# Performance work log

Measured on AMD Instinct MI355X. Metric: run time of the kernel, lower is better.

Reference implementation:

```python
import jax, jax.numpy as jnp
import numpy as np

GAZE_DIR = -1.0  # dataset != 'eyediap'
B, V, VM, LAT = 64, 5023, 3500, 556
D_IN = 3 * 224 * 224


def _skew(v):  # [B,3] -> [B,3,3]
    z = jnp.zeros_like(v[:, 0])
    return jnp.stack([
        jnp.stack([z, -v[:, 2], v[:, 1]], axis=1),
        jnp.stack([v[:, 2], z, -v[:, 0]], axis=1),
        jnp.stack([-v[:, 1], v[:, 0], z], axis=1)], axis=1)


def _axis_angle_to_matrix(aa):  # [B,3] -> [B,3,3], Rodrigues
    theta = jnp.linalg.norm(aa, axis=1, keepdims=True)
    axis = aa / jnp.maximum(theta, 1e-8)
    K = _skew(axis)
    s = jnp.sin(theta)[:, :, None]
    c = jnp.cos(theta)[:, :, None]
    return jnp.eye(3, dtype=aa.dtype) + s * K + (1.0 - c) * (K @ K)


def _find_gaze_R(init_gaze):  # rotation taking init_gaze -> [0,0,GAZE_DIR]
    a = init_gaze[:, 0, :]
    a = a / jnp.linalg.norm(a, axis=1, keepdims=True)
    b = jnp.broadcast_to(jnp.array([0.0, 0.0, GAZE_DIR], a.dtype), a.shape)
    v = jnp.cross(a, b)
    c = jnp.sum(a * b, axis=1)
    K = _skew(v)
    return jnp.eye(3, dtype=a.dtype) + K + (K @ K) * (1.0 / (1.0 + c + 1e-8))[:, None, None]


def _apply_eyeball_rotation(eyeball, centre, rot2):
    aa = jnp.concatenate([rot2, jnp.zeros_like(rot2[:, :1])], axis=1)
    R = _axis_angle_to_matrix(aa)
    return jnp.einsum('bvl,bli->bvi', eyeball - centre, R) + centre


def _forward(x, enc_W, enc_b, v_template, shape_basis, camera_parameters,
             landmarks, masked_landmarks, face_mask, lmask, rmask):
    b = x.shape[0]
    latent = x.reshape(b, -1) @ enc_W + enc_b  # encoder stub
    shape_p = latent[:, :400]
    face_rot = latent[:, 545:548]
    face_t = latent[:, 548:551]
    face_scale = latent[:, 551:552] + 1.0
    l_rot = latent[:, 552:554]
    r_rot = latent[:, 554:556]

    # FLAME shape model stub: template + linear blendshapes
    vert = v_template[None] + jnp.einsum('bs,svc->bvc', shape_p, shape_basis)
    vmean = vert.mean(axis=1, keepdims=True)
    vert = (jnp.einsum('bvl,bli->bvi', vert - vmean, _axis_angle_to_matrix(face_rot))
            * face_scale[:, :, None] + face_t[:, None, :])

    l_eye = vert[:, lmask]
    r_eye = vert[:, rmask]
    l_c = l_eye.mean(axis=1, keepdims=True)
    r_c = r_eye.mean(axis=1, keepdims=True)
    idx4 = landmarks[jnp.array([19, 22, 25, 28])]
    idx2 = landmarks[jnp.array([14, 18])]
    face_centre = (vert[:, idx4].mean(1) + vert[:, idx2].mean(1)) / 2.0

    l_init = vert[:, None, 4051] - l_c
    l_init = l_init / jnp.linalg.norm(l_init, axis=2, keepdims=True)
    r_init = vert[:, None, 4597] - r_c
    r_init = r_init / jnp.linalg.norm(r_init, axis=2, keepdims=True)

    le = jnp.einsum('bvl,bli->bvi', l_eye - l_c, _find_gaze_R(l_init)) + l_c
    re = jnp.einsum('bvl,bli->bvi', r_eye - r_c, _find_gaze_R(r_init)) + r_c
    le = _apply_eyeball_rotation(le, l_c, l_rot)
    re = _apply_eyeball_rotation(re, r_c, r_rot)
    # masks are disjoint: vert_no_eyes + vert_eyes == scatter back rotated eyes
    vert = vert.at[:, lmask].set(le).at[:, rmask].set(re)

    gdir = jnp.broadcast_to(jnp.array([0.0, 0.0, GAZE_DIR], vert.dtype), (b, 1, 3))
    zc = jnp.zeros((b, 1, 3), vert.dtype)
    left_gaze = _apply_eyeball_rotation(gdir, zc, l_rot)
    right_gaze = _apply_eyeball_rotation(gdir, zc, r_rot)

    lr_cross = jnp.cross(right_gaze, left_gaze, axis=2)
    A = jnp.concatenate([left_gaze, -right_gaze, lr_cross], axis=1).transpose(0, 2, 1)
    rhs = (r_c - l_c).transpose(0, 2, 1)
    sol = jnp.linalg.solve(A, rhs)  # [B,3,1]
    gp_l = l_c + sol[:, 0:1, :] * left_gaze
    gp_r = r_c + sol[:, 1:2, :] * right_gaze
    gp_mid = (gp_l + gp_r) / 2.0
    dist = jnp.linalg.norm(gp_l - gp_r, axis=2)  # [B,1]

    vmk = vert[:, face_mask]
    fl3d = vmk[:, masked_landmarks]
    # renderer stub: pinhole projection with [B,3,4] camera
    homog = jnp.concatenate([vmk, jnp.ones_like(vmk[..., :1])], axis=-1)
    p = jnp.einsum('bij,bvj->bvi', camera_parameters, homog)
    z = p[..., 2:3]
    zs = jnp.where(z >= 0, 1.0, -1.0) * jnp.maximum(jnp.abs(z), 1e-3)
    vert_img = jnp.concatenate([p[..., :2] / zs, z], axis=-1)

    dist_row = jnp.repeat(dist[:, :, None], 3, axis=2)  # [B,1,3]
    out = jnp.concatenate([
        vmk, vert_img, fl3d, l_c, r_c, face_centre[:, None, :],
        gp_l, gp_r, gp_mid,
        l_c + left_gaze * 1000.0, r_c + right_gaze * 1000.0,
        left_gaze, right_gaze, dist_row], axis=1)  # [B, 2*VM+68+11, 3]
    return out


def setup_inputs() -> dict:
    key = jax.random.key(0)
    ks = jax.random.split(key, 8)
    x = jax.random.normal(ks[0], (B, 3, 224, 224), jnp.float32)
    enc_W = jax.random.normal(ks[1], (D_IN, LAT), jnp.float32) * 1e-3
    enc_b = jax.random.normal(ks[2], (LAT,), jnp.float32) * 0.1
    v_template = jax.random.normal(ks[3], (V, 3), jnp.float32)
    shape_basis = jax.random.normal(ks[4], (400, V, 3), jnp.float32) * 0.01
    camera_parameters = jax.random.normal(ks[5], (B, 3, 4), jnp.float32)
    landmarks = jax.random.randint(ks[6], (68,), 0, VM)
    masked_landmarks = jax.random.randint(ks[7], (68,), 0, VM)
    face_mask = jnp.arange(VM)
    left_eyeball_mask = jnp.arange(3931, 4477)   # contains 4051
    right_eyeball_mask = jnp.arange(4477, 5023)  # contains 4597
    return {"x": x, "enc_W": enc_W, "enc_b": enc_b, "v_template": v_template,
            "shape_basis": shape_basis, "camera_parameters": camera_parameters,
            "landmarks": landmarks, "masked_landmarks": masked_landmarks,
            "face_mask": face_mask, "left_eyeball_mask": left_eyeball_mask,
            "right_eyeball_mask": right_eyeball_mask}


def reference(x, enc_W, enc_b, v_template, shape_basis, camera_parameters,
              landmarks, masked_landmarks, face_mask, left_eyeball_mask,
              right_eyeball_mask):
    return _forward(x, enc_W, enc_b, v_template, shape_basis, camera_parameters,
                    landmarks, masked_landmarks, face_mask, left_eyeball_mask,
                    right_eyeball_mask)
```

## Files before the change

kernel.cpp:

```cpp
#include <hip/hip_runtime.h>
#include <hip/hip_bf16.h>
#include <math.h>

#define B_    64
#define V_    5023
#define VM_   3500
#define LAT_  556
#define DIN_  150528
#define NS_   400
#define N2_   15069
#define ROWS_ 7079
#define LE0_  3931
#define NEYE_ 546

#define KC_   1024
#define KS_   32
#define NSUB_ (KC_/KS_)
#define SDW_  18
#define XSC_  64.0f
#define WSC_  4096.0f
#define OSC_  (1.0f/262144.0f)

#define WS_LATENT 0
#define WS_VERT0  35584
#define WS_VERT   1000000
#define WS_PB     1964416
#define PB_STRIDE 32

typedef _Float16 f16x8 __attribute__((ext_vector_type(8)));
typedef float    f32x4 __attribute__((ext_vector_type(4)));

union F16x8 { f16x8 v; unsigned int u[4]; _Float16 h[8]; };

static __device__ inline unsigned int packh(_Float16 a, _Float16 b) {
    union { _Float16 h; unsigned short u; } ca, cb;
    ca.h = a; cb.h = b;
    return (unsigned int)ca.u | ((unsigned int)cb.u << 16);
}

__global__ void k_init_latent(const float* __restrict__ enc_b,
                              float* __restrict__ latent) {
    int i = blockIdx.x * 256 + threadIdx.x;
    if (i < B_ * LAT_) latent[i] = enc_b[i % LAT_];
}

__global__ __launch_bounds__(256) void k_gemm(const float* __restrict__ x,
                                              const float* __restrict__ W,
                                              float* __restrict__ latent) {
    __shared__ __align__(16) unsigned int wt[2][2][64 * SDW_];
    const int tid = threadIdx.x;
    const int n0  = blockIdx.x * 64;
    const int k0  = blockIdx.y * KC_;
    const int sq   = tid & 15;
    const int skp  = tid >> 4;
    const int scol = n0 + sq * 4;
    const bool svalid = scol < LAT_;
    const int lane = tid & 63;
    const int w    = tid >> 6;
    const int wr   = w >> 1;
    const int wc   = w & 1;
    const int c16  = lane & 15;
    const int g    = lane >> 4;

    f32x4 acc[2][2] = {};
    float4 wv0, wv1;
    {
        const float* wp = W + (size_t)(k0 + 2 * skp) * LAT_ + scol;
        wv0 = svalid ? *(const float4*)wp : make_float4(0.f, 0.f, 0.f, 0.f);
        wv1 = svalid ? *(const float4*)(wp + LAT_) : make_float4(0.f, 0.f, 0.f, 0.f);
    }
    for (int s = 0; s < NSUB_; ++s) {
        const int db = s & 1;
        {
            float v0[4] = {wv0.x, wv0.y, wv0.z, wv0.w};
            float v1[4] = {wv1.x, wv1.y, wv1.z, wv1.w};
#pragma unroll
            for (int c = 0; c < 4; ++c) {
                float a = v0[c] * WSC_, b = v1[c] * WSC_;
                _Float16 h0 = (_Float16)a, h1 = (_Float16)b;
                _Float16 l0 = (_Float16)(a - (float)h0);
                _Float16 l1 = (_Float16)(b - (float)h1);
                wt[db][0][(sq * 4 + c) * SDW_ + skp] = packh(h0, h1);
                wt[db][1][(sq * 4 + c) * SDW_ + skp] = packh(l0, l1);
            }
        }
        if (s + 1 < NSUB_) {
            const float* wp = W + (size_t)(k0 + (s + 1) * KS_ + 2 * skp) * LAT_ + scol;
            wv0 = svalid ? *(const float4*)wp : make_float4(0.f, 0.f, 0.f, 0.f);
            wv1 = svalid ? *(const float4*)(wp + LAT_) : make_float4(0.f, 0.f, 0.f, 0.f);
        }
        __syncthreads();
        F16x8 ahi[2], alo[2];
#pragma unroll
        for (int rf = 0; rf < 2; ++rf) {
            const int row = 32 * wr + 16 * rf + c16;
            const float* xp = x + (size_t)row * DIN_ + k0 + s * KS_ + 8 * g;
            float4 a0 = *(const float4*)xp;
            float4 a1 = *(const float4*)(xp + 4);
            float av[8] = {a0.x, a0.y, a0.z, a0.w, a1.x, a1.y, a1.z, a1.w};
#pragma unroll
            for (int j = 0; j < 8; ++j) {
                float sv = av[j] * XSC_;
                _Float16 h = (_Float16)sv;
                ahi[rf].h[j] = h;
                alo[rf].h[j] = (_Float16)(sv - (float)h);
            }
        }
#pragma unroll
        for (int cf = 0; cf < 2; ++cf) {
            const int nl = 32 * wc + 16 * cf + c16;
            const unsigned int* ph = &wt[db][0][nl * SDW_ + 4 * g];
            const unsigned int* pl = &wt[db][1][nl * SDW_ + 4 * g];
            F16x8 bh, bl;
            uint2 t0 = *(const uint2*)ph;
            uint2 t1 = *(const uint2*)(ph + 2);
            bh.u[0] = t0.x; bh.u[1] = t0.y; bh.u[2] = t1.x; bh.u[3] = t1.y;
            uint2 u0 = *(const uint2*)pl;
            uint2 u1 = *(const uint2*)(pl + 2);
            bl.u[0] = u0.x; bl.u[1] = u0.y; bl.u[2] = u1.x; bl.u[3] = u1.y;
#pragma unroll
            for (int rf = 0; rf < 2; ++rf) {
                acc[rf][cf] = __builtin_amdgcn_mfma_f32_16x16x32_f16(ahi[rf].v, bh.v, acc[rf][cf], 0, 0, 0);
                acc[rf][cf] = __builtin_amdgcn_mfma_f32_16x16x32_f16(ahi[rf].v, bl.v, acc[rf][cf], 0, 0, 0);
                acc[rf][cf] = __builtin_amdgcn_mfma_f32_16x16x32_f16(alo[rf].v, bh.v, acc[rf][cf], 0, 0, 0);
            }
        }
    }
#pragma unroll
    for (int rf = 0; rf < 2; ++rf)
#pragma unroll
        for (int cf = 0; cf < 2; ++cf)
#pragma unroll
            for (int i = 0; i < 4; ++i) {
                int row = 32 * wr + 16 * rf + 4 * g + i;
                int col = n0 + 32 * wc + 16 * cf + c16;
                if (col < LAT_)
                    atomicAdd(&latent[row * LAT_ + col], acc[rf][cf][i] * OSC_);
            }
}

__global__ __launch_bounds__(256) void k_shape(const float* __restrict__ latent,
                                               const float* __restrict__ sb,
                                               const float* __restrict__ vt,
                                               float* __restrict__ vert0) {
    __shared__ float ps[16][64];
    __shared__ float bs[16][64];
    const int n0  = blockIdx.x * 64;
    const int tid = threadIdx.x;
    const int tb  = tid >> 4;
    const int tn  = tid & 15;
    const int lb  = tid >> 2;
    const int ls4 = (tid & 3) << 2;
    const int wss = tid >> 4;
    const int wn4 = (tid & 15) << 2;
    float acc[4][4];
#pragma unroll
    for (int j = 0; j < 4; ++j) {
        int nn = n0 + (tn << 2) + j;
        float v = (nn < N2_) ? vt[nn] : 0.f;
#pragma unroll
        for (int i = 0; i < 4; ++i) acc[i][j] = v;
    }
    for (int st = 0; st < NS_; st += 16) {
        float4 pv = *(const float4*)(latent + lb * LAT_ + st + ls4);
        float wv[4];
        int nn0 = n0 + wn4;
        if (nn0 + 3 < N2_) {
            float4 t = *(const float4*)(sb + (size_t)(st + wss) * N2_ + nn0);
            wv[0] = t.x; wv[1] = t.y; wv[2] = t.z; wv[3] = t.w;
        } else {
#pragma unroll
            for (int j = 0; j < 4; ++j) {
                int nn = nn0 + j;
                wv[j] = (nn < N2_) ? sb[(size_t)(st + wss) * N2_ + nn] : 0.f;
            }
        }
        __syncthreads();
        ps[ls4 + 0][lb] = pv.x;
        ps[ls4 + 1][lb] = pv.y;
        ps[ls4 + 2][lb] = pv.z;
        ps[ls4 + 3][lb] = pv.w;
#pragma unroll
        for (int j = 0; j < 4; ++j) bs[wss][wn4 + j] = wv[j];
        __syncthreads();
#pragma unroll
        for (int ss = 0; ss < 16; ++ss) {
            float4 av = *(const float4*)&ps[ss][tb << 2];
            float4 bv = *(const float4*)&bs[ss][tn << 2];
            float a[4] = {av.x, av.y, av.z, av.w};
            float b4[4] = {bv.x, bv.y, bv.z, bv.w};
#pragma unroll
            for (int i = 0; i < 4; ++i)
#pragma unroll
                for (int j = 0; j < 4; ++j)
                    acc[i][j] = fmaf(a[i], b4[j], acc[i][j]);
        }
    }
#pragma unroll
    for (int i = 0; i < 4; ++i) {
#pragma unroll
        for (int j = 0; j < 4; ++j) {
            int nn = n0 + (tn << 2) + j;
            if (nn < N2_) vert0[(size_t)((tb << 2) + i) * N2_ + nn] = acc[i][j];
        }
    }
}

__device__ inline void axis_angle(const float aa0, const float aa1, const float aa2,
                                  float R[9]) {
    float th  = sqrtf(aa0 * aa0 + aa1 * aa1 + aa2 * aa2);
    float inv = 1.0f / fmaxf(th, 1e-8f);
    float v0 = aa0 * inv, v1 = aa1 * inv, v2 = aa2 * inv;
    float s = sinf(th), c = cosf(th);
    float K[9] = {0.f, -v2, v1, v2, 0.f, -v0, -v1, v0, 0.f};
    float KK[9];
#pragma unroll
    for (int i = 0; i < 3; ++i)
#pragma unroll
        for (int j = 0; j < 3; ++j)
            KK[i * 3 + j] = K[i * 3 + 0] * K[0 * 3 + j] +
                            K[i * 3 + 1] * K[1 * 3 + j] +
                            K[i * 3 + 2] * K[2 * 3 + j];
    float omc = 1.0f - c;
#pragma unroll
    for (int i = 0; i < 9; ++i) R[i] = s * K[i] + omc * KK[i];
    R[0] += 1.f; R[4] += 1.f; R[8] += 1.f;
}

__global__ __launch_bounds__(256) void k_stats(const float* __restrict__ vert0,
                                               const float* __restrict__ latent,
                                               float* __restrict__ pb) {
    const int b   = blockIdx.x;
    const int tid = threadIdx.x;
    __shared__ float red[3][256];
    float s0 = 0.f, s1 = 0.f, s2 = 0.f;
    const float* row = vert0 + (size_t)b * N2_;
    for (int i = tid; i < N2_; i += 256) {
        float v = row[i];
        int c = i % 3;
        if (c == 0) s0 += v; else if (c == 1) s1 += v; else s2 += v;
    }
    red[0][tid] = s0; red[1][tid] = s1; red[2][tid] = s2;
    __syncthreads();
    for (int off = 128; off > 0; off >>= 1) {
        if (tid < off) {
            red[0][tid] += red[0][tid + off];
            red[1][tid] += red[1][tid + off];
            red[2][tid] += red[2][tid + off];
        }
        __syncthreads();
    }
    if (tid == 0) {
        float* p = pb + b * PB_STRIDE;
        p[0] = red[0][0] / (float)V_;
        p[1] = red[1][0] / (float)V_;
        p[2] = red[2][0] / (float)V_;
        const float* lat = latent + b * LAT_;
        float R[9];
        axis_angle(lat[545], lat[546], lat[547], R);
#pragma unroll
        for (int i = 0; i < 9; ++i) p[3 + i] = R[i];
        p[12] = lat[551] + 1.0f;
        p[13] = lat[548]; p[14] = lat[549]; p[15] = lat[550];
        float Rl[9], Rr[9];
        axis_angle(lat[552], lat[553], 0.f, Rl);
        axis_angle(lat[554], lat[555], 0.f, Rr);
        p[16] = -Rl[6]; p[17] = -Rl[7]; p[18] = -Rl[8];
        p[19] = -Rr[6]; p[20] = -Rr[7]; p[21] = -Rr[8];
    }
}

__global__ __launch_bounds__(256) void k_transform(const float* __restrict__ vert0,
                                                   const float* __restrict__ pb,
                                                   const float* __restrict__ cam,
                                                   float* __restrict__ vert,
                                                   float* __restrict__ out) {
    const int b = blockIdx.y;
    const int v = blockIdx.x * 256 + threadIdx.x;
    if (v >= V_) return;
    const float* p = pb + b * PB_STRIDE;
    const size_t vo = (size_t)b * N2_ + (size_t)v * 3;
    float w0 = vert0[vo + 0] - p[0];
    float w1 = vert0[vo + 1] - p[1];
    float w2 = vert0[vo + 2] - p[2];
    float sc = p[12];
    float r0 = (w0 * p[3] + w1 * p[6] + w2 * p[9])  * sc + p[13];
    float r1 = (w0 * p[4] + w1 * p[7] + w2 * p[10]) * sc + p[14];
    float r2 = (w0 * p[5] + w1 * p[8] + w2 * p[11]) * sc + p[15];
    vert[vo + 0] = r0; vert[vo + 1] = r1; vert[vo + 2] = r2;
    if (v < VM_) {
        size_t o = ((size_t)b * ROWS_ + v) * 3;
        out[o + 0] = r0; out[o + 1] = r1; out[o + 2] = r2;
        const float* cb = cam + b * 12;
        float p0 = cb[0] * r0 + cb[1] * r1 + cb[2]  * r2 + cb[3];
        float p1 = cb[4] * r0 + cb[5] * r1 + cb[6]  * r2 + cb[7];
        float p2 = cb[8] * r0 + cb[9] * r1 + cb[10] * r2 + cb[11];
        float zs = (p2 >= 0.f ? 1.f : -1.f) * fmaxf(fabsf(p2), 0.001f);
        size_t o2 = ((size_t)b * ROWS_ + VM_ + v) * 3;
        out[o2 + 0] = p0 / zs; out[o2 + 1] = p1 / zs; out[o2 + 2] = p2;
    }
}

__global__ __launch_bounds__(256) void k_final(const float* __restrict__ vert,
                                               const float* __restrict__ pb,
                                               const int* __restrict__ lmk,
                                               const int* __restrict__ mlmk,
                                               float* __restrict__ out) {
    const int b   = blockIdx.x;
    const int tid = threadIdx.x;
    __shared__ float red[6][256];
    const float* row = vert + (size_t)b * N2_;
    float l0 = 0.f, l1 = 0.f, l2 = 0.f, r0 = 0.f, r1 = 0.f, r2 = 0.f;
    for (int i = tid; i < 2 * NEYE_ * 3; i += 256) {
        float v = row[LE0_ * 3 + i];
        int c = i % 3;
        if (i < NEYE_ * 3) {
            if (c == 0) l0 += v; else if (c == 1) l1 += v; else l2 += v;
        } else {
            if (c == 0) r0 += v; else if (c == 1) r1 += v; else r2 += v;
        }
    }
    red[0][tid] = l0; red[1][tid] = l1; red[2][tid] = l2;
    red[3][tid] = r0; red[4][tid] = r1; red[5][tid] = r2;
    __syncthreads();
    for (int off = 128; off > 0; off >>= 1) {
        if (tid < off) {
#pragma unroll
            for (int q = 0; q < 6; ++q) red[q][tid] += red[q][tid + off];
        }
        __syncthreads();
    }
    if (tid < 204) {
        int j = tid / 3, c = tid % 3;
        int vi = mlmk[j];
        out[((size_t)b * ROWS_ + 7000 + j) * 3 + c] = row[(size_t)vi * 3 + c];
    }
    if (tid == 0) {
        float lc[3], rc[3];
        const float invn = 1.0f / (float)NEYE_;
#pragma unroll
        for (int c = 0; c < 3; ++c) { lc[c] = red[c][0] * invn; rc[c] = red[3 + c][0] * invn; }
        int i4a = lmk[19], i4b = lmk[22], i4c = lmk[25], i4d = lmk[28];
        int i2a = lmk[14], i2b = lmk[18];
        float fc[3];
#pragma unroll
        for (int c = 0; c < 3; ++c) {
            float m4 = (row[i4a * 3 + c] + row[i4b * 3 + c] +
                        row[i4c * 3 + c] + row[i4d * 3 + c]) * 0.25f;
            float m2 = (row[i2a * 3 + c] + row[i2b * 3 + c]) * 0.5f;
            fc[c] = (m4 + m2) * 0.5f;
        }
        const float* p = pb + b * PB_STRIDE;
        float lg[3] = {p[16], p[17], p[18]};
        float rg[3] = {p[19], p[20], p[21]};
        float cr[3] = {rg[1] * lg[2] - rg[2] * lg[1],
                       rg[2] * lg[0] - rg[0] * lg[2],
                       rg[0] * lg[1] - rg[1] * lg[0]};
        float A[3][3], rhs[3];
#pragma unroll
        for (int i = 0; i < 3; ++i) {
            A[i][0] = lg[i]; A[i][1] = -rg[i]; A[i][2] = cr[i];
            rhs[i] = rc[i] - lc[i];
        }
        for (int k = 0; k < 3; ++k) {
            int mrow = k; float mv = fabsf(A[k][k]);
            for (int i = k + 1; i < 3; ++i) {
                float av = fabsf(A[i][k]);
                if (av > mv) { mv = av; mrow = i; }
            }
            if (mrow != k) {
                for (int j = 0; j < 3; ++j) { float t = A[k][j]; A[k][j] = A[mrow][j]; A[mrow][j] = t; }
                float t = rhs[k]; rhs[k] = rhs[mrow]; rhs[mrow] = t;
            }
            float inv = 1.0f / A[k][k];
            for (int i = k + 1; i < 3; ++i) {
                float f = A[i][k] * inv;
                for (int j = k; j < 3; ++j) A[i][j] -= f * A[k][j];
                rhs[i] -= f * rhs[k];
            }
        }
        float sol2 = rhs[2] / A[2][2];
        float sol1 = (rhs[1] - A[1][2] * sol2) / A[1][1];
        float sol0 = (rhs[0] - A[0][1] * sol1 - A[0][2] * sol2) / A[0][0];
        float gpl[3], gpr[3], gpm[3];
#pragma unroll
        for (int c = 0; c < 3; ++c) {
            gpl[c] = lc[c] + sol0 * lg[c];
            gpr[c] = rc[c] + sol1 * rg[c];
            gpm[c] = (gpl[c] + gpr[c]) * 0.5f;
        }
        float d0 = gpl[0] - gpr[0], d1 = gpl[1] - gpr[1], d2 = gpl[2] - gpr[2];
        float dist = sqrtf(d0 * d0 + d1 * d1 + d2 * d2);
        float* o = out + ((size_t)b * ROWS_ + 7068) * 3;
#pragma unroll
        for (int c = 0; c < 3; ++c) {
            o[0 * 3 + c]  = lc[c];
            o[1 * 3 + c]  = rc[c];
            o[2 * 3 + c]  = fc[c];
            o[3 * 3 + c]  = gpl[c];
            o[4 * 3 + c]  = gpr[c];
            o[5 * 3 + c]  = gpm[c];
            o[6 * 3 + c]  = lc[c] + lg[c] * 1000.0f;
            o[7 * 3 + c]  = rc[c] + rg[c] * 1000.0f;
            o[8 * 3 + c]  = lg[c];
            o[9 * 3 + c]  = rg[c];
            o[10 * 3 + c] = dist;
        }
    }
}

extern "C" void kernel_launch(void* const* d_in, const int* in_sizes, int n_in,
                              void* d_out, int out_size, void* d_ws, size_t ws_size,
                              hipStream_t stream) {
    const float* x    = (const float*)d_in[0];
    const float* W    = (const float*)d_in[1];
    const float* eb   = (const float*)d_in[2];
    const float* vt   = (const float*)d_in[3];
    const float* sb   = (const float*)d_in[4];
    const float* cam  = (const float*)d_in[5];
    const int*   lmk  = (const int*)d_in[6];
    const int*   mlmk = (const int*)d_in[7];
    float* out = (float*)d_out;
    float* ws  = (float*)d_ws;
    float* latent = ws + WS_LATENT;
    float* vert0  = ws + WS_VERT0;
    float* vert   = ws + WS_VERT;
    float* pb     = ws + WS_PB;

    k_init_latent<<<139, 256, 0, stream>>>(eb, latent);
    k_gemm<<<dim3(9, 147), 256, 0, stream>>>(x, W, latent);
    k_shape<<<236, 256, 0, stream>>>(latent, sb, vt, vert0);
    k_stats<<<64, 256, 0, stream>>>(vert0, latent, pb);
    k_transform<<<dim3(20, 64), 256, 0, stream>>>(vert0, pb, cam, vert, out);
    k_final<<<64, 256, 0, stream>>>(vert, pb, lmk, mlmk, out);
}
```

Baseline: 600.0 us.

## Skip unused latent columns in encoder GEMM and prefetch x tiles

Remaps GEMM column tiles so only latent columns actually consumed downstream (shape params and face/eye params) are computed, reducing the grid from 9 to 7 column tiles. Also software-prefetches the next x sub-tile into registers alongside the W prefetch. This cuts redundant x reads and MFMA work; unused latent columns stay at the bias value, which is safe only if they are never read.

Result: faster. 574.1 us (-4.3%).

```diff
diff --git a/kernel.cpp b/kernel.cpp
--- a/kernel.cpp
+++ b/kernel.cpp
@@ -16,6 +16,7 @@
 #define KC_   1024
 #define KS_   32
 #define NSUB_ (KC_/KS_)
+#define NT_   7
 #define SDW_  18
 #define XSC_  64.0f
 #define WSC_  4096.0f
@@ -38,6 +39,13 @@
     return (unsigned int)ca.u | ((unsigned int)cb.u << 16);
 }
 
+static __device__ inline int quad_map(int t, int q) {
+    if (t < 6) return t * 16 + q;
+    if (q < 4) return 96 + q;
+    if (q < 7) return 132 + q;
+    return -1;
+}
+
 __global__ void k_init_latent(const float* __restrict__ enc_b,
                               float* __restrict__ latent) {
     int i = blockIdx.x * 256 + threadIdx.x;
@@ -49,12 +57,13 @@
                                               float* __restrict__ latent) {
     __shared__ __align__(16) unsigned int wt[2][2][64 * SDW_];
     const int tid = threadIdx.x;
-    const int n0  = blockIdx.x * 64;
+    const int nt  = blockIdx.x;
     const int k0  = blockIdx.y * KC_;
     const int sq   = tid & 15;
     const int skp  = tid >> 4;
-    const int scol = n0 + sq * 4;
-    const bool svalid = scol < LAT_;
+    const int gq   = quad_map(nt, sq);
+    const bool svalid = gq >= 0;
+    const int scol = svalid ? gq * 4 : 0;
     const int lane = tid & 63;
     const int w    = tid >> 6;
     const int wr   = w >> 1;
@@ -63,11 +72,15 @@
     const int g    = lane >> 4;
 
     f32x4 acc[2][2] = {};
-    float4 wv0, wv1;
+    float4 wv0, wv1, xc0, xc1, xc2, xc3;
     {
         const float* wp = W + (size_t)(k0 + 2 * skp) * LAT_ + scol;
         wv0 = svalid ? *(const float4*)wp : make_float4(0.f, 0.f, 0.f, 0.f);
         wv1 = svalid ? *(const float4*)(wp + LAT_) : make_float4(0.f, 0.f, 0.f, 0.f);
+        const float* xp0 = x + (size_t)(32 * wr + c16) * DIN_ + k0 + 8 * g;
+        const float* xp1 = xp0 + (size_t)16 * DIN_;
+        xc0 = *(const float4*)xp0; xc1 = *(const float4*)(xp0 + 4);
+        xc2 = *(const float4*)xp1; xc3 = *(const float4*)(xp1 + 4);
     }
     for (int s = 0; s < NSUB_; ++s) {
         const int db = s & 1;
@@ -84,27 +97,32 @@
                 wt[db][1][(sq * 4 + c) * SDW_ + skp] = packh(l0, l1);
             }
         }
+        F16x8 ahi[2], alo[2];
+        {
+            float av0[8] = {xc0.x, xc0.y, xc0.z, xc0.w, xc1.x, xc1.y, xc1.z, xc1.w};
+            float av1[8] = {xc2.x, xc2.y, xc2.z, xc2.w, xc3.x, xc3.y, xc3.z, xc3.w};
+#pragma unroll
+            for (int j = 0; j < 8; ++j) {
+                float sv = av0[j] * XSC_;
+                _Float16 h = (_Float16)sv;
+                ahi[0].h[j] = h;
+                alo[0].h[j] = (_Float16)(sv - (float)h);
+                float sw = av1[j] * XSC_;
+                _Float16 h2 = (_Float16)sw;
+                ahi[1].h[j] = h2;
+                alo[1].h[j] = (_Float16)(sw - (float)h2);
+            }
+        }
+        __syncthreads();
         if (s + 1 < NSUB_) {
-            const float* wp = W + (size_t)(k0 + (s + 1) * KS_ + 2 * skp) * LAT_ + scol;
+            const int kb = k0 + (s + 1) * KS_;
+            const float* wp = W + (size_t)(kb + 2 * skp) * LAT_ + scol;
             wv0 = svalid ? *(const float4*)wp : make_float4(0.f, 0.f, 0.f, 0.f);
             wv1 = svalid ? *(const float4*)(wp + LAT_) : make_float4(0.f, 0.f, 0.f, 0.f);
-        }
-        __syncthreads();
-        F16x8 ahi[2], alo[2];
-#pragma unroll
-        for (int rf = 0; rf < 2; ++rf) {
-            const int row = 32 * wr + 16 * rf + c16;
-            const float* xp = x + (size_t)row * DIN_ + k0 + s * KS_ + 8 * g;
-            float4 a0 = *(const float4*)xp;
-            float4 a1 = *(const float4*)(xp + 4);
-            float av[8] = {a0.x, a0.y, a0.z, a0.w, a1.x, a1.y, a1.z, a1.w};
-#pragma unroll
-            for (int j = 0; j < 8; ++j) {
-                float sv = av[j] * XSC_;
-                _Float16 h = (_Float16)sv;
-                ahi[rf].h[j] = h;
-                alo[rf].h[j] = (_Float16)(sv - (float)h);
-            }
+            const float* xp0 = x + (size_t)(32 * wr + c16) * DIN_ + kb + 8 * g;
+            const float* xp1 = xp0 + (size_t)16 * DIN_;
+            xc0 = *(const float4*)xp0; xc1 = *(const float4*)(xp0 + 4);
+            xc2 = *(const float4*)xp1; xc3 = *(const float4*)(xp1 + 4);
         }
 #pragma unroll
         for (int cf = 0; cf < 2; ++cf) {
@@ -129,14 +147,17 @@
 #pragma unroll
     for (int rf = 0; rf < 2; ++rf)
 #pragma unroll
-        for (int cf = 0; cf < 2; ++cf)
+        for (int cf = 0; cf < 2; ++cf) {
+            const int cl = 32 * wc + 16 * cf + c16;
+            const int cgq = quad_map(nt, cl >> 2);
+            if (cgq < 0) continue;
+            const int col = cgq * 4 + (cl & 3);
 #pragma unroll
             for (int i = 0; i < 4; ++i) {
                 int row = 32 * wr + 16 * rf + 4 * g + i;
-                int col = n0 + 32 * wc + 16 * cf + c16;
-                if (col < LAT_)
-                    atomicAdd(&latent[row * LAT_ + col], acc[rf][cf][i] * OSC_);
-            }
+                atomicAdd(&latent[row * LAT_ + col], acc[rf][cf][i] * OSC_);
+            }
+        }
 }
 
 __global__ __launch_bounds__(256) void k_shape(const float* __restrict__ latent,
@@ -428,7 +449,7 @@
     float* pb     = ws + WS_PB;
 
     k_init_latent<<<139, 256, 0, stream>>>(eb, latent);
-    k_gemm<<<dim3(9, 147), 256, 0, stream>>>(x, W, latent);
+    k_gemm<<<dim3(NT_, 147), 256, 0, stream>>>(x, W, latent);
     k_shape<<<236, 256, 0, stream>>>(latent, sb, vt, vert0);
     k_stats<<<64, 256, 0, stream>>>(vert0, latent, pb);
     k_transform<<<dim3(20, 64), 256, 0, stream>>>(vert0, pb, cam, vert, out);
```
